# Optimization experiments

Measured on AMD Instinct MI355X. Metric: run time of the kernel, lower is better.

Reference implementation:

```python
import jax, jax.numpy as jnp
import numpy as np

N_HEAD = 16
N_EMBD = 1024
HEAD_DIM = N_EMBD // N_HEAD


def setup_inputs() -> dict:
    key = jax.random.key(0)
    k1, k2, k3 = jax.random.split(key, 3)
    B, T, C = 4, 2048, N_EMBD
    scale = 1.0 / np.sqrt(C)
    x = jax.random.normal(k1, (B, T, C), dtype=jnp.float32)
    W_attn = jax.random.normal(k2, (C, 3 * C), dtype=jnp.float32) * scale
    W_proj = jax.random.normal(k3, (C, C), dtype=jnp.float32) * scale
    return {"x": x, "W_attn": W_attn, "W_proj": W_proj}


def reference(x, W_attn, W_proj):
    B, T, C = x.shape
    H, D = N_HEAD, HEAD_DIM
    qkv = x @ W_attn  # [B,T,3C]
    q, k, v = jnp.split(qkv, 3, axis=-1)
    # [B,H,T,D]
    q = q.reshape(B, T, H, D).transpose(0, 2, 1, 3)
    k = k.reshape(B, T, H, D).transpose(0, 2, 1, 3)
    v = v.reshape(B, T, H, D).transpose(0, 2, 1, 3)
    att = jnp.einsum("bhqd,bhkd->bhqk", q, k) * (1.0 / np.sqrt(D))
    mask = jnp.tril(jnp.ones((T, T), dtype=bool))
    att = jnp.where(mask, att, -jnp.inf)
    att = jax.nn.softmax(att, axis=-1)
    y = jnp.einsum("bhqk,bhkd->bhqd", att, v)
    y = y.transpose(0, 2, 1, 3).reshape(B, T, C)
    return y @ W_proj
```

## Files before the change

kernel.cpp:

```cpp
#include <hip/hip_runtime.h>
#include <hip/hip_bf16.h>

typedef __bf16 bf16x8 __attribute__((ext_vector_type(8)));
typedef __bf16 bf16x4 __attribute__((ext_vector_type(4)));
typedef float  f32x4  __attribute__((ext_vector_type(4)));

#define MFMA16(A, B, C) __builtin_amdgcn_mfma_f32_16x16x32_bf16((A), (B), (C), 0, 0, 0)

static constexpr int TB = 4;
static constexpr int TT = 2048;
static constexpr int TC = 1024;
static constexpr int TH = 16;
static constexpr int TD = 64;
static constexpr int TM = TB * TT;

__device__ __forceinline__ void gload16(const __bf16* g, __bf16* l) {
  __builtin_amdgcn_global_load_lds(
      (const __attribute__((address_space(1))) unsigned int*)g,
      (__attribute__((address_space(3))) unsigned int*)l, 16, 0, 0);
}

__global__ __launch_bounds__(256) void k_convert(const float* __restrict__ in,
                                                 __bf16* __restrict__ out, int n4) {
  int stride = gridDim.x * blockDim.x;
  for (int i = blockIdx.x * blockDim.x + threadIdx.x; i < n4; i += stride) {
    float4 v = *(const float4*)(in + (size_t)i * 4);
    bf16x4 o;
    o[0] = (__bf16)v.x; o[1] = (__bf16)v.y; o[2] = (__bf16)v.z; o[3] = (__bf16)v.w;
    *(bf16x4*)(out + (size_t)i * 4) = o;
  }
}

__global__ __launch_bounds__(256) void k_transpose_w(const float* __restrict__ w,
                                                     __bf16* __restrict__ wt,
                                                     int K, int N) {
  __shared__ __align__(16) __bf16 tile[64][72];
  const int k0 = blockIdx.y * 64, n0 = blockIdx.x * 64;
  const int tid = threadIdx.x;
#pragma unroll
  for (int it = 0; it < 4; ++it) {
    int c = tid + it * 256;
    int row = c >> 4, cc = (c & 15) * 4;
    float4 v = *(const float4*)(w + (size_t)(k0 + row) * N + n0 + cc);
    tile[row][cc + 0] = (__bf16)v.x;
    tile[row][cc + 1] = (__bf16)v.y;
    tile[row][cc + 2] = (__bf16)v.z;
    tile[row][cc + 3] = (__bf16)v.w;
  }
  __syncthreads();
#pragma unroll
  for (int it = 0; it < 2; ++it) {
    int c = tid + it * 256;
    int n = c >> 3, kk = (c & 7) * 8;
    bf16x8 v;
#pragma unroll
    for (int j = 0; j < 8; ++j) v[j] = tile[kk + j][n];
    *(bf16x8*)(wt + (size_t)(n0 + n) * K + k0 + kk) = v;
  }
}

template <int EPI>
__global__ __launch_bounds__(256, 3) void k_gemm(const __bf16* __restrict__ A,
                                                 const __bf16* __restrict__ Bt,
                                                 int N, float* __restrict__ outf,
                                                 __bf16* __restrict__ Qo,
                                                 __bf16* __restrict__ Ko,
                                                 __bf16* __restrict__ Vto) {
  __shared__ __align__(16) __bf16 As[128 * 64];
  __shared__ __align__(16) __bf16 Bs[128 * 64];
  const int gx = gridDim.x;
  const int nwg = gx * gridDim.y;
  int id = blockIdx.y * gx + blockIdx.x;
  id = (id & 7) * (nwg >> 3) + (id >> 3);
  const int bm = id / gx, bn = id % gx;
  const int tid = threadIdx.x, lane = tid & 63, wid = tid >> 6;
  const int wr = wid >> 1, wc = wid & 1;
  const int lr = lane & 15, lg = lane >> 4;

  f32x4 acc[4][4];
  const f32x4 zero = {0.f, 0.f, 0.f, 0.f};
#pragma unroll
  for (int mi = 0; mi < 4; ++mi)
#pragma unroll
    for (int ni = 0; ni < 4; ++ni) acc[mi][ni] = zero;

  const __bf16* Ab = A + (size_t)bm * 128 * 1024;
  const __bf16* Bb = Bt + (size_t)bn * 128 * 1024;

  const int rr = wid * 8 + (lane >> 3);
  const int sc = (lane & 7) ^ (lane >> 3);

  int offA[4][2], offB[4][2];
#pragma unroll
  for (int i = 0; i < 4; ++i)
#pragma unroll
    for (int kk = 0; kk < 2; ++kk) {
      const int xo = ((((kk << 2) + lg) ^ (lr & 7)) << 3);
      offA[i][kk] = (wr * 64 + i * 16 + lr) * 64 + xo;
      offB[i][kk] = (wc * 64 + i * 16 + lr) * 64 + xo;
    }

  for (int k0 = 0; k0 < 1024; k0 += 64) {
#pragma unroll
    for (int it = 0; it < 4; ++it) {
      const int r = it * 32 + rr;
      gload16(Ab + (size_t)r * 1024 + k0 + sc * 8, As + it * 2048 + wid * 512);
      gload16(Bb + (size_t)r * 1024 + k0 + sc * 8, Bs + it * 2048 + wid * 512);
    }
    __syncthreads();

    bf16x8 af[4][2], bfr[4][2];
#pragma unroll
    for (int mi = 0; mi < 4; ++mi)
#pragma unroll
      for (int kk = 0; kk < 2; ++kk) {
        af[mi][kk]  = *(const bf16x8*)&As[offA[mi][kk]];
        bfr[mi][kk] = *(const bf16x8*)&Bs[offB[mi][kk]];
      }
#pragma unroll
    for (int mi = 0; mi < 4; ++mi)
#pragma unroll
      for (int ni = 0; ni < 4; ++ni) {
        acc[mi][ni] = MFMA16(af[mi][0], bfr[ni][0], acc[mi][ni]);
        acc[mi][ni] = MFMA16(af[mi][1], bfr[ni][1], acc[mi][ni]);
      }
    __syncthreads();
  }

  const int rb = bm * 128 + wr * 64 + lg * 4;
  const int cb = bn * 128 + wc * 64 + lr;
  if constexpr (EPI == 0) {
#pragma unroll
    for (int mi = 0; mi < 4; ++mi)
#pragma unroll
      for (int ni = 0; ni < 4; ++ni)
#pragma unroll
        for (int j = 0; j < 4; ++j)
          outf[(size_t)(rb + mi * 16 + j) * N + cb + ni * 16] = acc[mi][ni][j];
  } else {
    const int which = (bn * 128) >> 10;
    if (which == 2) {
#pragma unroll
      for (int mi = 0; mi < 4; ++mi) {
        const int r0 = rb + mi * 16;
        const int b = r0 >> 11, t0 = r0 & 2047;
#pragma unroll
        for (int ni = 0; ni < 4; ++ni) {
          const int c = cb + ni * 16;
          const int h = (c & 1023) >> 6, d = c & 63;
          bf16x4 pk;
#pragma unroll
          for (int j = 0; j < 4; ++j) pk[j] = (__bf16)acc[mi][ni][j];
          *(bf16x4*)(Vto + (((size_t)(b * TH + h) * TD + d) * TT) + t0) = pk;
        }
      }
    } else {
#pragma unroll
      for (int mi = 0; mi < 4; ++mi) {
#pragma unroll
        for (int ni = 0; ni < 4; ++ni) {
#pragma unroll
          for (int j = 0; j < 4; ++j) {
            float v = acc[mi][ni][j];
            int r = rb + mi * 16 + j;
            int c = cb + ni * 16;
            int within = c & 1023;
            int h = within >> 6, d = within & 63;
            int b = r >> 11, t = r & 2047;
            size_t idx = (((size_t)(b * TH + h)) * TT + t) * TD + d;
            if (which == 0)
              Qo[idx] = (__bf16)(v * 0.18033688f);
            else
              Ko[idx] = (__bf16)v;
          }
        }
      }
    }
  }
}

__global__ __launch_bounds__(256, 3) void k_attn(const __bf16* __restrict__ Qg,
                                                 const __bf16* __restrict__ Kg,
                                                 const __bf16* __restrict__ Vt,
                                                 __bf16* __restrict__ Y) {
  __shared__ __align__(16) __bf16 Ksh[2][64 * 64];
  __shared__ __align__(16) __bf16 Vsh[2][64 * 64];
  __shared__ __align__(16) __bf16 Plds[4][16][64];
  const int flat = blockIdx.x + (blockIdx.y << 4);
  const int W = (flat & 7) * 128 + (flat >> 3);
  const int bh = W >> 4, p = W & 15;
  const int tid = threadIdx.x, lane = tid & 63, w = tid >> 6;
  const int lr = lane & 15, lg = lane >> 4, lg8 = lg << 3, lg4 = lg << 2;

  const __bf16* Qb = Qg + ((size_t)bh * TT) * TD;
  const __bf16* Kb = Kg + ((size_t)bh * TT) * TD;
  const __bf16* Vb = Vt + ((size_t)bh * TD) * TT;
  const int b = bh >> 4, hh = bh & 15;
  __bf16* Yb = Y + ((size_t)b * TT) * TC + hh * TD;

  const int c0 = p, c1 = 31 - p;
  const int nkt0 = c0 + 1;
  const int nt = nkt0 + c1 + 1;

  const f32x4 zero = {0.f, 0.f, 0.f, 0.f};

  auto STAGE = [&](int bb, int kb) {
#pragma unroll
    for (int it = 0; it < 2; ++it) {
      int slot = tid + (it << 8);
      int r = slot >> 3;
      int sc = (slot & 7) ^ (r & 7);
      gload16(Kb + (size_t)(kb + r) * TD + sc * 8, &Ksh[bb][(it << 11) + (w << 9)]);
      gload16(Vb + (size_t)r * TT + kb + sc * 8, &Vsh[bb][(it << 11) + (w << 9)]);
    }
  };

  int off[4][2];
#pragma unroll
  for (int i = 0; i < 4; ++i)
#pragma unroll
    for (int h = 0; h < 2; ++h)
      off[i][h] = (i * 16 + lr) * 64 + ((((h << 2) + lg) ^ (lr & 7)) << 3);

  int wOff[4];
#pragma unroll
  for (int kf = 0; kf < 4; ++kf)
    wOff[kf] = ((((kf << 1) + (lg >> 1)) ^ (lr & 7)) << 3) + ((lg & 1) << 2);
  const int rOff0 = (lg ^ (lr & 7)) << 3;
  const int rOff1 = ((4 + lg) ^ (lr & 7)) << 3;

  int qw = c0 * 64 + w * 16;
  bf16x8 qf[2];
#pragma unroll
  for (int h = 0; h < 2; ++h)
    qf[h] = *(const bf16x8*)(Qb + (size_t)(qw + lr) * TD + h * 32 + lg8);
  f32x4 o[4];
  f32x4 l4 = zero;
#pragma unroll
  for (int df = 0; df < 4; ++df) o[df] = zero;

  auto epilogue = [&]() {
    float L = (l4[0] + l4[1]) + (l4[2] + l4[3]);
    L += __shfl_xor(L, 16);
    L += __shfl_xor(L, 32);
    const float inv = 1.0f / L;
#pragma unroll
    for (int j = 0; j < 4; ++j) {
      const float invr = __shfl(inv, lg4 + j);
      const int row = qw + lg4 + j;
#pragma unroll
      for (int df = 0; df < 4; ++df)
        Yb[(size_t)row * TC + df * 16 + lr] = (__bf16)(o[df][j] * invr);
    }
  };

  int cur = 0;
  STAGE(0, 0);
  __syncthreads();

  for (int t = 0; t < nt; ++t) {
    if (t + 1 < nt) {
      int t2 = t + 1;
      int kb2 = (t2 < nkt0 ? t2 : t2 - nkt0) << 6;
      STAGE(cur ^ 1, kb2);
    }
    if (t == nkt0) {
      epilogue();
      qw = c1 * 64 + w * 16;
#pragma unroll
      for (int h = 0; h < 2; ++h)
        qf[h] = *(const bf16x8*)(Qb + (size_t)(qw + lr) * TD + h * 32 + lg8);
      l4 = zero;
#pragma unroll
      for (int df = 0; df < 4; ++df) o[df] = zero;
    }

    const int kb = (t < nkt0 ? t : t - nkt0) << 6;
    const __bf16* Kt = Ksh[cur];
    const __bf16* Vst = Vsh[cur];

    bf16x8 kA[4][2];
#pragma unroll
    for (int kf = 0; kf < 4; ++kf)
#pragma unroll
      for (int h = 0; h < 2; ++h)
        kA[kf][h] = *(const bf16x8*)&Kt[off[kf][h]];

    f32x4 s4[4];
    __builtin_amdgcn_s_setprio(1);
#pragma unroll
    for (int kf = 0; kf < 4; ++kf) {
      f32x4 z = zero;
      z = MFMA16(kA[kf][0], qf[0], z);
      z = MFMA16(kA[kf][1], qf[1], z);
      s4[kf] = z;
    }
    __builtin_amdgcn_s_setprio(0);

    bf16x8 vB[4][2];
#pragma unroll
    for (int df = 0; df < 4; ++df)
#pragma unroll
      for (int h = 0; h < 2; ++h)
        vB[df][h] = *(const bf16x8*)&Vst[off[df][h]];

    {
      const int q = qw + lr;
      const bool diag = (kb + 63 > qw);
#pragma unroll
      for (int kf = 0; kf < 4; ++kf) {
#pragma unroll
        for (int j = 0; j < 4; ++j) {
          float arg = s4[kf][j];
          if (diag) {
            int key = kb + kf * 16 + lg4 + j;
            if (key > q) arg = -16384.0f;
          }
          s4[kf][j] = __builtin_amdgcn_exp2f(arg);
        }
        l4 += s4[kf];
        bf16x4 pk;
#pragma unroll
        for (int j = 0; j < 4; ++j) pk[j] = (__bf16)s4[kf][j];
        *(bf16x4*)&Plds[w][lr][wOff[kf]] = pk;
      }
    }

    __builtin_amdgcn_s_setprio(1);
    {
      bf16x8 pa0 = *(const bf16x8*)&Plds[w][lr][rOff0];
      bf16x8 pa1 = *(const bf16x8*)&Plds[w][lr][rOff1];
#pragma unroll
      for (int df = 0; df < 4; ++df) {
        o[df] = MFMA16(pa0, vB[df][0], o[df]);
        o[df] = MFMA16(pa1, vB[df][1], o[df]);
      }
    }
    __builtin_amdgcn_s_setprio(0);

    __syncthreads();
    cur ^= 1;
  }

  epilogue();
}

extern "C" void kernel_launch(void* const* d_in, const int* in_sizes, int n_in,
                              void* d_out, int out_size, void* d_ws, size_t ws_size,
                              hipStream_t stream) {
  const float* x  = (const float*)d_in[0];
  const float* Wa = (const float*)d_in[1];
  const float* Wp = (const float*)d_in[2];
  float* out = (float*)d_out;

  char* ws = (char*)d_ws;
  size_t off = 0;
  auto alloc = [&](size_t bytes) { char* p = ws + off; off += bytes; return p; };
  __bf16* xb   = (__bf16*)alloc((size_t)TM * TC * 2);
  __bf16* wat  = (__bf16*)alloc((size_t)3 * TC * TC * 2);
  __bf16* wpt  = (__bf16*)alloc((size_t)TC * TC * 2);
  __bf16* Qb   = (__bf16*)alloc((size_t)TM * TC * 2);
  __bf16* Kb   = (__bf16*)alloc((size_t)TM * TC * 2);
  __bf16* Vtb  = (__bf16*)alloc((size_t)TM * TC * 2);
  __bf16* Yb   = xb;

  k_convert<<<2048, 256, 0, stream>>>(x, xb, (TM * TC) / 4);
  k_transpose_w<<<dim3(48, 16), 256, 0, stream>>>(Wa, wat, 1024, 3072);
  k_transpose_w<<<dim3(16, 16), 256, 0, stream>>>(Wp, wpt, 1024, 1024);
  k_gemm<1><<<dim3(24, 64), 256, 0, stream>>>(xb, wat, 3072, nullptr, Qb, Kb, Vtb);
  k_attn<<<dim3(16, 64), 256, 0, stream>>>(Qb, Kb, Vtb, Yb);
  k_gemm<0><<<dim3(8, 64), 256, 0, stream>>>(Yb, wpt, 1024, out, nullptr, nullptr, nullptr);
}
```

Baseline: 162.9 us.

## Share K/V tiles across both causal query tiles in one key loop

Rewrites the attention loop so each block walks the key range once and computes scores for both of its paired query tiles (c0 and c1) from the same staged K/V tile. The c0 tile is only processed while its causal range is active. This removes the duplicate staging and LDS reads of the first c0+1 key tiles and the mid-loop epilogue/Q reload. In exchange it keeps two sets of Q fragments, accumulators and row sums live, raising register pressure, and reuses the per-wave P buffer for both tiles in one iteration.

```diff
diff --git a/kernel.cpp b/kernel.cpp
--- a/kernel.cpp
+++ b/kernel.cpp
@@ -199,8 +199,9 @@
   __bf16* Yb = Y + ((size_t)b * TT) * TC + hh * TD;
 
   const int c0 = p, c1 = 31 - p;
-  const int nkt0 = c0 + 1;
-  const int nt = nkt0 + c1 + 1;
+  const int nt = c1 + 1;
+  const int qw0 = c0 * 64 + w * 16;
+  const int qw1 = c1 * 64 + w * 16;
 
   const f32x4 zero = {0.f, 0.f, 0.f, 0.f};
 
@@ -229,17 +230,18 @@
   const int rOff0 = (lg ^ (lr & 7)) << 3;
   const int rOff1 = ((4 + lg) ^ (lr & 7)) << 3;
 
-  int qw = c0 * 64 + w * 16;
-  bf16x8 qf[2];
-#pragma unroll
-  for (int h = 0; h < 2; ++h)
-    qf[h] = *(const bf16x8*)(Qb + (size_t)(qw + lr) * TD + h * 32 + lg8);
-  f32x4 o[4];
-  f32x4 l4 = zero;
-#pragma unroll
-  for (int df = 0; df < 4; ++df) o[df] = zero;
-
-  auto epilogue = [&]() {
+  bf16x8 qf0[2], qf1[2];
+#pragma unroll
+  for (int h = 0; h < 2; ++h) {
+    qf0[h] = *(const bf16x8*)(Qb + (size_t)(qw0 + lr) * TD + h * 32 + lg8);
+    qf1[h] = *(const bf16x8*)(Qb + (size_t)(qw1 + lr) * TD + h * 32 + lg8);
+  }
+  f32x4 o0[4], o1[4];
+  f32x4 l0 = zero, l1 = zero;
+#pragma unroll
+  for (int df = 0; df < 4; ++df) { o0[df] = zero; o1[df] = zero; }
+
+  auto epilogue = [&](int qw, f32x4 (&o)[4], f32x4& l4) {
     float L = (l4[0] + l4[1]) + (l4[2] + l4[3]);
     L += __shfl_xor(L, 16);
     L += __shfl_xor(L, 32);
@@ -259,25 +261,12 @@
   __syncthreads();
 
   for (int t = 0; t < nt; ++t) {
-    if (t + 1 < nt) {
-      int t2 = t + 1;
-      int kb2 = (t2 < nkt0 ? t2 : t2 - nkt0) << 6;
-      STAGE(cur ^ 1, kb2);
-    }
-    if (t == nkt0) {
-      epilogue();
-      qw = c1 * 64 + w * 16;
-#pragma unroll
-      for (int h = 0; h < 2; ++h)
-        qf[h] = *(const bf16x8*)(Qb + (size_t)(qw + lr) * TD + h * 32 + lg8);
-      l4 = zero;
-#pragma unroll
-      for (int df = 0; df < 4; ++df) o[df] = zero;
-    }
-
-    const int kb = (t < nkt0 ? t : t - nkt0) << 6;
+    if (t + 1 < nt) STAGE(cur ^ 1, (t + 1) << 6);
+
+    const int kb = t << 6;
     const __bf16* Kt = Ksh[cur];
     const __bf16* Vst = Vsh[cur];
+    const bool act0 = (t <= c0);
 
     bf16x8 kA[4][2];
 #pragma unroll
@@ -286,42 +275,85 @@
       for (int h = 0; h < 2; ++h)
         kA[kf][h] = *(const bf16x8*)&Kt[off[kf][h]];
 
-    f32x4 s4[4];
+    f32x4 s4a[4], s4b[4];
     __builtin_amdgcn_s_setprio(1);
 #pragma unroll
     for (int kf = 0; kf < 4; ++kf) {
       f32x4 z = zero;
-      z = MFMA16(kA[kf][0], qf[0], z);
-      z = MFMA16(kA[kf][1], qf[1], z);
-      s4[kf] = z;
+      z = MFMA16(kA[kf][0], qf1[0], z);
+      z = MFMA16(kA[kf][1], qf1[1], z);
+      s4b[kf] = z;
+    }
+    if (act0) {
+#pragma unroll
+      for (int kf = 0; kf < 4; ++kf) {
+        f32x4 z = zero;
+        z = MFMA16(kA[kf][0], qf0[0], z);
+        z = MFMA16(kA[kf][1], qf0[1], z);
+        s4a[kf] = z;
+      }
     }
     __builtin_amdgcn_s_setprio(0);
 
-    bf16x8 vB[4][2];
-#pragma unroll
-    for (int df = 0; df < 4; ++df)
-#pragma unroll
-      for (int h = 0; h < 2; ++h)
-        vB[df][h] = *(const bf16x8*)&Vst[off[df][h]];
-
-    {
-      const int q = qw + lr;
-      const bool diag = (kb + 63 > qw);
+    if (act0) {
+      const int q = qw0 + lr;
+      const bool diag = (kb + 63 > qw0);
 #pragma unroll
       for (int kf = 0; kf < 4; ++kf) {
 #pragma unroll
         for (int j = 0; j < 4; ++j) {
-          float arg = s4[kf][j];
+          float arg = s4a[kf][j];
           if (diag) {
             int key = kb + kf * 16 + lg4 + j;
             if (key > q) arg = -16384.0f;
           }
-          s4[kf][j] = __builtin_amdgcn_exp2f(arg);
+          s4a[kf][j] = __builtin_amdgcn_exp2f(arg);
         }
-        l4 += s4[kf];
+        l0 += s4a[kf];
         bf16x4 pk;
 #pragma unroll
-        for (int j = 0; j < 4; ++j) pk[j] = (__bf16)s4[kf][j];
+        for (int j = 0; j < 4; ++j) pk[j] = (__bf16)s4a[kf][j];
+        *(bf16x4*)&Plds[w][lr][wOff[kf]] = pk;
+      }
+    }
+
+    bf16x8 vB[4][2];
+#pragma unroll
+    for (int df = 0; df < 4; ++df)
+#pragma unroll
+      for (int h = 0; h < 2; ++h)
+        vB[df][h] = *(const bf16x8*)&Vst[off[df][h]];
+
+    if (act0) {
+      __builtin_amdgcn_s_setprio(1);
+      bf16x8 pa0 = *(const bf16x8*)&Plds[w][lr][rOff0];
+      bf16x8 pa1 = *(const bf16x8*)&Plds[w][lr][rOff1];
+#pragma unroll
+      for (int df = 0; df < 4; ++df) {
+        o0[df] = MFMA16(pa0, vB[df][0], o0[df]);
+        o0[df] = MFMA16(pa1, vB[df][1], o0[df]);
+      }
+      __builtin_amdgcn_s_setprio(0);
+    }
+
+    {
+      const int q = qw1 + lr;
+      const bool diag = (kb + 63 > qw1);
+#pragma unroll
+      for (int kf = 0; kf < 4; ++kf) {
+#pragma unroll
+        for (int j = 0; j < 4; ++j) {
+          float arg = s4b[kf][j];
+          if (diag) {
+            int key = kb + kf * 16 + lg4 + j;
+            if (key > q) arg = -16384.0f;
+          }
+          s4b[kf][j] = __builtin_amdgcn_exp2f(arg);
+        }
+        l1 += s4b[kf];
+        bf16x4 pk;
+#pragma unroll
+        for (int j = 0; j < 4; ++j) pk[j] = (__bf16)s4b[kf][j];
         *(bf16x4*)&Plds[w][lr][wOff[kf]] = pk;
       }
     }
@@ -332,8 +364,8 @@
       bf16x8 pa1 = *(const bf16x8*)&Plds[w][lr][rOff1];
 #pragma unroll
       for (int df = 0; df < 4; ++df) {
-        o[df] = MFMA16(pa0, vB[df][0], o[df]);
-        o[df] = MFMA16(pa1, vB[df][1], o[df]);
+        o1[df] = MFMA16(pa0, vB[df][0], o1[df]);
+        o1[df] = MFMA16(pa1, vB[df][1], o1[df]);
       }
     }
     __builtin_amdgcn_s_setprio(0);
@@ -342,7 +374,8 @@
     cur ^= 1;
   }
 
-  epilogue();
+  epilogue(qw0, o0, l0);
+  epilogue(qw1, o1, l1);
 }
 
 extern "C" void kernel_launch(void* const* d_in, const int* in_sizes, int n_in,
```

Result: slower. 175.2 us (+7.5%).
